# Performance work log

Measured on AMD Instinct MI355X. Metric: run time of the kernel, lower is better.

Reference implementation:

```python
import jax, jax.numpy as jnp
import numpy as np


def _laplacian_kernel(x, z, bandwidth):
    x_sq = jnp.sum(x * x, axis=-1, keepdims=True)          # [N, 1]
    z_sq = jnp.sum(z * z, axis=-1)[None, :]                # [1, M]
    d2 = x_sq + z_sq - 2.0 * jnp.einsum('nd,md->nm', x, z)  # [N, M]
    d = jnp.sqrt(jnp.maximum(d2, 0.0))
    return jnp.exp(-d / bandwidth)


def setup_inputs() -> dict:
    key = jax.random.key(0)
    k1, k2, k3 = jax.random.split(key, 3)
    N, M, D, Y = 8192, 20000, 1024, 256
    batch = jax.random.normal(k1, (N, D), dtype=jnp.float32)
    centers = jax.random.normal(k2, (M, D), dtype=jnp.float32)
    weight = jax.random.normal(k3, (M, Y), dtype=jnp.float32) * 0.02
    return {"batch": batch, "centers": centers, "weight": weight, "bandwidth": 10}


def reference(batch, centers, weight, bandwidth):
    kmat = _laplacian_kernel(batch, centers, float(bandwidth))  # [N, M]
    pred = kmat @ weight                                        # [N, Y]
    return pred
```

## Files before the change

kernel.cpp:

```cpp
#include <hip/hip_runtime.h>
#include <stdint.h>

#define N_ROWS 8192
#define D_DIM  1024
#define M_CENT 20000
#define M_PAD  20224
#define M_TILES 79
#define Y_DIM  256
#define BM 64
#define BN 256
#define BK 32
#define NCHUNK 32
#define MSPLIT 8
#define TILES_PER_SPLIT 10
#define LDSP_STRIDE 264

#define BUFE 10240
#define ZOFFE 2048
#define POFF 20480

typedef __attribute__((ext_vector_type(4))) float  f32x4;
typedef __attribute__((ext_vector_type(8))) __bf16 bf16x8;

__device__ __forceinline__ unsigned short f2bf(float f) {
    union { float f; unsigned u; } v; v.f = f;
    unsigned u = v.u;
    u += 0x7FFFu + ((u >> 16) & 1u);
    return (unsigned short)(u >> 16);
}

__device__ __forceinline__ void gll16(void* lds, const void* g) {
    __builtin_amdgcn_global_load_lds(
        (const __attribute__((address_space(1))) void*)g,
        (__attribute__((address_space(3))) void*)lds, 16, 0, 0);
}

__global__ void cast_rows_kernel(const float* __restrict__ src,
                                 unsigned short* __restrict__ dst,
                                 float* __restrict__ sq, int nrows_valid) {
    int row = blockIdx.x;
    int t = threadIdx.x;
    float s = 0.f;
    if (row < nrows_valid) {
        float4 v = ((const float4*)(src + (size_t)row * D_DIM))[t];
        s = v.x * v.x + v.y * v.y + v.z * v.z + v.w * v.w;
        ushort4 o;
        o.x = f2bf(v.x); o.y = f2bf(v.y); o.z = f2bf(v.z); o.w = f2bf(v.w);
        ((ushort4*)(dst + (size_t)row * D_DIM))[t] = o;
    } else {
        ((ushort4*)(dst + (size_t)row * D_DIM))[t] = make_ushort4(0, 0, 0, 0);
    }
    __shared__ float red[4];
    for (int off = 32; off; off >>= 1) s += __shfl_down(s, off, 64);
    if ((t & 63) == 0) red[t >> 6] = s;
    __syncthreads();
    if (t == 0) sq[row] = red[0] + red[1] + red[2] + red[3];
}

__global__ void cast_wT_kernel(const float* __restrict__ w,
                               unsigned short* __restrict__ wT) {
    __shared__ float tile[32][33];
    int k0 = blockIdx.x * 32;
    int y0 = blockIdx.y * 32;
    int tx = threadIdx.x & 31;
    int ty = threadIdx.x >> 5;
    #pragma unroll
    for (int i = 0; i < 4; ++i) {
        int k = k0 + ty + i * 8;
        float v = (k < M_CENT) ? w[(size_t)k * Y_DIM + y0 + tx] : 0.f;
        tile[tx][ty + i * 8] = v;
    }
    __syncthreads();
    #pragma unroll
    for (int i = 0; i < 4; ++i) {
        int yl = ty + i * 8;
        wT[(size_t)(y0 + yl) * M_PAD + k0 + tx] = f2bf(tile[yl][tx]);
    }
}


#define STAGE(PAR, M0, KBASE) do {                                            \
    { int lin_ = t; int row_ = lin_ >> 2, c_ = lin_ & 3;    \
      gll16(&lds_all[(PAR) * BUFE + lin_ * 8],                                \
            Xb + (size_t)(row0 + row_) * D_DIM + (KBASE) +                    \
                ((c_ ^ ((row_ >> 1) & 3)) * 8)); }                            \
    _Pragma("unroll")                                                         \
    for (int i_ = 0; i_ < 4; ++i_) {                       \
        int lin_ = t + i_ * 256;                                              \
        int row_ = lin_ >> 2, c_ = lin_ & 3;                                  \
        gll16(&lds_all[(PAR) * BUFE + ZOFFE + lin_ * 8],                      \
              Zb + (size_t)((M0) + row_) * D_DIM + (KBASE) +                  \
                  ((c_ ^ ((row_ >> 1) & 3)) * 8));                            \
    } } while (0)

#define CHUNK(PAR, M0N, KBN) do {                                             \
    asm volatile("" ::: "memory");                                            \
    __builtin_amdgcn_s_barrier();                  \
    asm volatile("" ::: "memory");                                            \
    STAGE(PAR ^ 1, M0N, KBN);                                                 \
    __builtin_amdgcn_sched_barrier(0);                                        \
    asm volatile("s_waitcnt vmcnt(5)" ::: "memory");      \
    __builtin_amdgcn_s_barrier();            \
    asm volatile("" ::: "memory");                                            \
    bf16x8 a_[4], b_[4];                                                      \
    _Pragma("unroll")                                                         \
    for (int it_ = 0; it_ < 4; ++it_)                                         \
        a_[it_] = *(const bf16x8*)&lds_all[(PAR) * BUFE +                     \
            (it_ * 16 + l16) * BK + swl];                                     \
    _Pragma("unroll")                                                         \
    for (int jt_ = 0; jt_ < 4; ++jt_)                                         \
        b_[jt_] = *(const bf16x8*)&lds_all[(PAR) * BUFE + ZOFFE +             \
            (wave * 64 + jt_ * 16 + l16) * BK + swl];                         \
    __builtin_amdgcn_s_setprio(1);                                            \
    _Pragma("unroll")                                                         \
    for (int it_ = 0; it_ < 4; ++it_)                                         \
        _Pragma("unroll")                                                     \
        for (int jt_ = 0; jt_ < 4; ++jt_)                                     \
            S[it_ * 4 + jt_] = __builtin_amdgcn_mfma_f32_16x16x32_bf16(       \
                a_[it_], b_[jt_], S[it_ * 4 + jt_], 0, 0, 0);                 \
    __builtin_amdgcn_s_setprio(0);                                            \
  } while (0)

__global__ void __launch_bounds__(256, 2)
fused_kernel(const unsigned short* __restrict__ Xb,
             const unsigned short* __restrict__ Zb,
             const unsigned short* __restrict__ WbT,
             const float* __restrict__ xsq,
             const float* __restrict__ zsq,
             const int* __restrict__ bwp,
             float* __restrict__ out) {
    __shared__ unsigned short lds_all[POFF + BM * LDSP_STRIDE];
    __shared__ float lds_xsq[BM];
    __shared__ float lds_zsq[BN];

    const int t    = threadIdx.x;
    const int wave = t >> 6;
    const int lane = t & 63;
    const int quad = lane >> 4;
    const int l16  = lane & 15;
    const int swl  = (quad ^ ((l16 >> 1) & 3)) * 8;

    const int row0 = blockIdx.x * BM;
    const int mt0  = blockIdx.y * TILES_PER_SPLIT;
    int mt_end = mt0 + TILES_PER_SPLIT;
    if (mt_end > M_TILES) mt_end = M_TILES;

    int bwi = *bwp;
    float bw;
    if (bwi > 0 && bwi < 1000000) bw = (float)bwi;
    else { union { int i; float f; } u; u.i = bwi; bw = u.f; }
    const float inv_bw = 1.0f / bw;

    if (t < BM) lds_xsq[t] = xsq[row0 + t];
    asm volatile("s_waitcnt lgkmcnt(0)" ::: "memory");

    const f32x4 vzero = {0.f, 0.f, 0.f, 0.f};
    f32x4 Oacc[16];
    #pragma unroll
    for (int i = 0; i < 16; ++i) Oacc[i] = vzero;

    STAGE(0, mt0 * BN, 0);
    __builtin_amdgcn_sched_barrier(0);

    for (int mt = mt0; mt < mt_end; ++mt) {
        const int m0 = mt * BN;
        const int m0next = (mt + 1 < mt_end) ? m0 + BN : m0;

        lds_zsq[t] = zsq[m0 + t];
        asm volatile("s_waitcnt lgkmcnt(0)" ::: "memory");

        f32x4 S[16];
        #pragma unroll
        for (int i = 0; i < 16; ++i) S[i] = vzero;

        #pragma unroll 1
        for (int kc = 0; kc < NCHUNK; kc += 2) {
            const bool last = (kc + 2 == NCHUNK);
            CHUNK(0, m0, (kc + 1) * BK);
            CHUNK(1, last ? m0next : m0, last ? 0 : (kc + 2) * BK);
        }

        #pragma unroll
        for (int it = 0; it < 4; ++it) {
            #pragma unroll
            for (int jt = 0; jt < 4; ++jt) {
                f32x4 s4 = S[it * 4 + jt];
                const int col = wave * 64 + jt * 16 + l16;
                const float zq = lds_zsq[col];
                #pragma unroll
                for (int r = 0; r < 4; ++r) {
                    const int row = it * 16 + quad * 4 + r;
                    float d2 = lds_xsq[row] + zq - 2.0f * s4[r];
                    d2 = fmaxf(d2, 0.f);
                    float d;
                    asm("v_sqrt_f32 %0, %1" : "=v"(d) : "v"(d2));
                    float p = __expf(-d * inv_bw);
                    lds_all[POFF + row * LDSP_STRIDE + col] = f2bf(p);
                }
            }
        }
        asm volatile("s_waitcnt lgkmcnt(0)" ::: "memory");
        __builtin_amdgcn_s_barrier();
        asm volatile("" ::: "memory");

        #pragma unroll
        for (int ks = 0; ks < 8; ++ks) {
            const int koff = ks * 32 + quad * 8;
            bf16x8 a[4], b[4];
            #pragma unroll
            for (int rt = 0; rt < 4; ++rt)
                a[rt] = *(const bf16x8*)&lds_all[POFF +
                    (rt * 16 + l16) * LDSP_STRIDE + koff];
            #pragma unroll
            for (int ct = 0; ct < 4; ++ct) {
                const int y = wave * 64 + ct * 16 + l16;
                b[ct] = *(const bf16x8*)(WbT + (size_t)y * M_PAD + m0 + koff);
            }
            __builtin_amdgcn_s_setprio(1);
            #pragma unroll
            for (int rt = 0; rt < 4; ++rt)
                #pragma unroll
                for (int ct = 0; ct < 4; ++ct)
                    Oacc[rt * 4 + ct] = __builtin_amdgcn_mfma_f32_16x16x32_bf16(
                        a[rt], b[ct], Oacc[rt * 4 + ct], 0, 0, 0);
            __builtin_amdgcn_s_setprio(0);
        }
    }

    asm volatile("s_waitcnt vmcnt(0)" ::: "memory");

    #pragma unroll
    for (int rt = 0; rt < 4; ++rt) {
        #pragma unroll
        for (int ct = 0; ct < 4; ++ct) {
            f32x4 v = Oacc[rt * 4 + ct];
            const int y = wave * 64 + ct * 16 + l16;
            #pragma unroll
            for (int r = 0; r < 4; ++r) {
                const int row = row0 + rt * 16 + quad * 4 + r;
                atomicAdd(&out[(size_t)row * Y_DIM + y], v[r]);
            }
        }
    }
}

extern "C" void kernel_launch(void* const* d_in, const int* in_sizes, int n_in,
                              void* d_out, int out_size, void* d_ws, size_t ws_size,
                              hipStream_t stream) {
    const float* X = (const float*)d_in[0];
    const float* Z = (const float*)d_in[1];
    const float* W = (const float*)d_in[2];
    const int*  bw = (const int*)d_in[3];
    float* out = (float*)d_out;

    char* ws = (char*)d_ws;
    size_t off = 0;
    unsigned short* Xb  = (unsigned short*)(ws + off); off += (size_t)N_ROWS * D_DIM * 2;
    unsigned short* Zb  = (unsigned short*)(ws + off); off += (size_t)M_PAD * D_DIM * 2;
    unsigned short* WbT = (unsigned short*)(ws + off); off += (size_t)Y_DIM * M_PAD * 2;
    float* xsq = (float*)(ws + off); off += (size_t)N_ROWS * 4;
    float* zsq = (float*)(ws + off); off += (size_t)M_PAD * 4;

    hipMemsetAsync(d_out, 0, (size_t)out_size * sizeof(float), stream);
    cast_rows_kernel<<<N_ROWS, 256, 0, stream>>>(X, Xb, xsq, N_ROWS);
    cast_rows_kernel<<<M_PAD, 256, 0, stream>>>(Z, Zb, zsq, M_CENT);
    cast_wT_kernel<<<dim3(M_PAD / 32, Y_DIM / 32), 256, 0, stream>>>(W, WbT);
    fused_kernel<<<dim3(N_ROWS / BM, MSPLIT), 256, 0, stream>>>(
        Xb, Zb, WbT, xsq, zsq, bw, out);
}
```

Before: 774.7 us.

## Use four-buffer LDS ring with prefetch distance two and one barrier per chunk

Replaces the double-buffered K-chunk staging with a four-slot LDS ring that prefetches two chunks ahead. This removes the leading barrier in each chunk and loosens the vmcnt wait, so more global-to-LDS traffic is in flight while MFMAs run. The P tile and the x/z squared-norm arrays now share the larger LDS allocation with the ring buffers. The norm loads move to after the distance GEMM, and an end-of-tile barrier is added to guard against overlap. The cost is more LDS per block and a riskier buffer-aliasing scheme.

```diff
diff --git a/kernel.cpp b/kernel.cpp
--- a/kernel.cpp
+++ b/kernel.cpp
@@ -18,6 +18,8 @@
 #define BUFE 10240
 #define ZOFFE 2048
 #define POFF 20480
+#define XGOFF 37376
+#define ZGOFF 37504
 
 typedef __attribute__((ext_vector_type(4))) float  f32x4;
 typedef __attribute__((ext_vector_type(8))) __bf16 bf16x8;
@@ -79,37 +81,35 @@
 }
 
 
-#define STAGE(PAR, M0, KBASE) do {                                            \
+#define STAGE(BUF, M0, KBASE) do {                                            \
     { int lin_ = t; int row_ = lin_ >> 2, c_ = lin_ & 3;    \
-      gll16(&lds_all[(PAR) * BUFE + lin_ * 8],                                \
+      gll16(&lds_all[(BUF) * BUFE + lin_ * 8],                                \
             Xb + (size_t)(row0 + row_) * D_DIM + (KBASE) +                    \
                 ((c_ ^ ((row_ >> 1) & 3)) * 8)); }                            \
     _Pragma("unroll")                                                         \
     for (int i_ = 0; i_ < 4; ++i_) {                       \
         int lin_ = t + i_ * 256;                                              \
         int row_ = lin_ >> 2, c_ = lin_ & 3;                                  \
-        gll16(&lds_all[(PAR) * BUFE + ZOFFE + lin_ * 8],                      \
+        gll16(&lds_all[(BUF) * BUFE + ZOFFE + lin_ * 8],                      \
               Zb + (size_t)((M0) + row_) * D_DIM + (KBASE) +                  \
                   ((c_ ^ ((row_ >> 1) & 3)) * 8));                            \
     } } while (0)
 
-#define CHUNK(PAR, M0N, KBN) do {                                             \
+#define CHUNK(RD, ST, M0S, KBS) do {                                          \
     asm volatile("" ::: "memory");                                            \
-    __builtin_amdgcn_s_barrier();                  \
-    asm volatile("" ::: "memory");                                            \
-    STAGE(PAR ^ 1, M0N, KBN);                                                 \
+    STAGE(ST, M0S, KBS);                                                      \
     __builtin_amdgcn_sched_barrier(0);                                        \
-    asm volatile("s_waitcnt vmcnt(5)" ::: "memory");      \
-    __builtin_amdgcn_s_barrier();            \
+    asm volatile("s_waitcnt vmcnt(10)" ::: "memory");     \
+    __builtin_amdgcn_s_barrier();              \
     asm volatile("" ::: "memory");                                            \
     bf16x8 a_[4], b_[4];                                                      \
     _Pragma("unroll")                                                         \
     for (int it_ = 0; it_ < 4; ++it_)                                         \
-        a_[it_] = *(const bf16x8*)&lds_all[(PAR) * BUFE +                     \
+        a_[it_] = *(const bf16x8*)&lds_all[(RD) * BUFE +                      \
             (it_ * 16 + l16) * BK + swl];                                     \
     _Pragma("unroll")                                                         \
     for (int jt_ = 0; jt_ < 4; ++jt_)                                         \
-        b_[jt_] = *(const bf16x8*)&lds_all[(PAR) * BUFE + ZOFFE +             \
+        b_[jt_] = *(const bf16x8*)&lds_all[(RD) * BUFE + ZOFFE +              \
             (wave * 64 + jt_ * 16 + l16) * BK + swl];                         \
     __builtin_amdgcn_s_setprio(1);                                            \
     _Pragma("unroll")                                                         \
@@ -129,9 +129,9 @@
              const float* __restrict__ zsq,
              const int* __restrict__ bwp,
              float* __restrict__ out) {
-    __shared__ unsigned short lds_all[POFF + BM * LDSP_STRIDE];
-    __shared__ float lds_xsq[BM];
-    __shared__ float lds_zsq[BN];
+    __shared__ unsigned short lds_all[4 * BUFE];
+    float* xg = (float*)&lds_all[XGOFF];
+    float* zg = (float*)&lds_all[ZGOFF];
 
     const int t    = threadIdx.x;
     const int wave = t >> 6;
@@ -151,34 +151,41 @@
     else { union { int i; float f; } u; u.i = bwi; bw = u.f; }
     const float inv_bw = 1.0f / bw;
 
-    if (t < BM) lds_xsq[t] = xsq[row0 + t];
-    asm volatile("s_waitcnt lgkmcnt(0)" ::: "memory");
-
     const f32x4 vzero = {0.f, 0.f, 0.f, 0.f};
     f32x4 Oacc[16];
     #pragma unroll
     for (int i = 0; i < 16; ++i) Oacc[i] = vzero;
 
     STAGE(0, mt0 * BN, 0);
+    STAGE(1, mt0 * BN, BK);
     __builtin_amdgcn_sched_barrier(0);
 
     for (int mt = mt0; mt < mt_end; ++mt) {
         const int m0 = mt * BN;
         const int m0next = (mt + 1 < mt_end) ? m0 + BN : m0;
 
-        lds_zsq[t] = zsq[m0 + t];
+        f32x4 S[16];
+        #pragma unroll
+        for (int i = 0; i < 16; ++i) S[i] = vzero;
+
+        #pragma unroll 1
+        for (int kc = 0; kc < NCHUNK; kc += 4) {
+            const bool tl = (kc == NCHUNK - 4);
+            CHUNK(0, 2, m0, (kc + 2) * BK);
+            CHUNK(1, 3, m0, (kc + 3) * BK);
+            CHUNK(2, 0, tl ? m0next : m0, tl ? 0 : (kc + 4) * BK);
+            CHUNK(3, 1, tl ? m0next : m0, tl ? BK : (kc + 5) * BK);
+        }
+
+        {
+            float tZ = zsq[m0 + t];
+            float tX = (t < BM) ? xsq[row0 + t] : 0.f;
+            zg[t] = tZ;
+            if (t < BM) xg[t] = tX;
+        }
         asm volatile("s_waitcnt lgkmcnt(0)" ::: "memory");
-
-        f32x4 S[16];
-        #pragma unroll
-        for (int i = 0; i < 16; ++i) S[i] = vzero;
-
-        #pragma unroll 1
-        for (int kc = 0; kc < NCHUNK; kc += 2) {
-            const bool last = (kc + 2 == NCHUNK);
-            CHUNK(0, m0, (kc + 1) * BK);
-            CHUNK(1, last ? m0next : m0, last ? 0 : (kc + 2) * BK);
-        }
+        __builtin_amdgcn_s_barrier();
+        asm volatile("" ::: "memory");
 
         #pragma unroll
         for (int it = 0; it < 4; ++it) {
@@ -186,11 +193,11 @@
             for (int jt = 0; jt < 4; ++jt) {
                 f32x4 s4 = S[it * 4 + jt];
                 const int col = wave * 64 + jt * 16 + l16;
-                const float zq = lds_zsq[col];
+                const float zq = zg[col];
                 #pragma unroll
                 for (int r = 0; r < 4; ++r) {
                     const int row = it * 16 + quad * 4 + r;
-                    float d2 = lds_xsq[row] + zq - 2.0f * s4[r];
+                    float d2 = xg[row] + zq - 2.0f * s4[r];
                     d2 = fmaxf(d2, 0.f);
                     float d;
                     asm("v_sqrt_f32 %0, %1" : "=v"(d) : "v"(d2));
@@ -225,6 +232,10 @@
                         a[rt], b[ct], Oacc[rt * 4 + ct], 0, 0, 0);
             __builtin_amdgcn_s_setprio(0);
         }
+
+        asm volatile("" ::: "memory");
+        __builtin_amdgcn_s_barrier();
+        asm volatile("" ::: "memory");
     }
 
     asm volatile("s_waitcnt vmcnt(0)" ::: "memory");
```

New measurement: 795.0 us. 2.6% more time.
